# Optimization experiments

Measured on AMD Instinct MI355X. Metric: run time of the kernel, lower is better.

The kernel has to match this reference:

```python
import jax, jax.numpy as jnp
import numpy as np

TEMPERATURE = 0.75
SINKHORN_ITERS = 7
EPS = 1e-6
R_THRESH = 1e-3


def setup_inputs() -> dict:
    key = jax.random.key(0)
    k1, k2, k3, k4 = jax.random.split(key, 4)
    b, h, t, d = 1, 8, 2048, 64
    n = 32  # uniform buckets of size t // n = 64
    q = jax.random.normal(k1, (b, h, t, d), jnp.float32)
    k_ = jax.random.normal(k2, (b, h, t, d), jnp.float32)
    v = jax.random.normal(k3, (b, h, t, d), jnp.float32)
    gumbel_u = jax.random.uniform(k4, (b * h, n, n), jnp.float32)
    return {"q": q, "k": k_, "v": v, "gumbel_u": gumbel_u, "num_buckets": n}


def _sort_net_R(qm, km, gumbel_u, d):
    # qm, km: [bh, n, s, d] -> bucket sums [bh, n, d]
    q_sums = qm.sum(axis=2)
    k_sums = km.sum(axis=2)
    logits = jnp.einsum('bie,bje->bij', q_sums, k_sums) * (d ** -0.5)
    # gumbel_sinkhorn(relu(logits))
    r = jnp.log(jax.nn.relu(logits) + EPS)
    g = -jnp.log(-jnp.log(gumbel_u + EPS) + EPS)
    r = (r + g) / TEMPERATURE
    for _ in range(SINKHORN_ITERS):
        r = r - jax.nn.logsumexp(r, axis=2, keepdims=True)
        r = r - jax.nn.logsumexp(r, axis=1, keepdims=True)
    return jnp.exp(r)  # [bh, n, n]


def reference(q, k, v, gumbel_u, num_buckets):
    b, h, t, d = q.shape
    bh = b * h
    n = num_buckets
    s = t // n  # uniform bucket size
    qm = q.reshape(bh, n, s, d)
    km = k.reshape(bh, n, s, d)
    vm = v.reshape(bh, n, s, d)

    R = _sort_net_R(qm, km, gumbel_u, d)
    # torch skips pairs with R_ij <= 1e-3 (output is zero); multiply by masked R
    Rm = jnp.where(R > R_THRESH, R, 0.0)

    scale = d ** -0.5
    # keys for pair (i, j) are concat(k_i, k_j): split score into self + cross
    S_self = jnp.einsum('bise,bite->bist', qm, km) * scale          # [bh,n,s,s]
    S_cross = jnp.einsum('bise,bjte->bijst', qm, km) * scale        # [bh,n,n,s,s]
    scores = jnp.concatenate(
        [jnp.broadcast_to(S_self[:, :, None], (bh, n, n, s, s)), S_cross],
        axis=-1)                                                    # [bh,n,n,s,2s]
    w = jax.nn.softmax(scores, axis=-1)
    w_i, w_j = w[..., :s], w[..., s:]
    # out_ij = (w_i @ v_i + w_j @ v_j) * R_ij, summed over j
    out = (jnp.einsum('bijst,bite,bij->bise', w_i, vm, Rm)
           + jnp.einsum('bijst,bjte,bij->bise', w_j, vm, Rm))       # [bh,n,s,d]
    return out.reshape(b, h, t, d)
```

## Files before the change

kernel.cpp:

```cpp
#include <hip/hip_runtime.h>
#include <math.h>
#include <stdint.h>

#define BH 8
#define NB 32
#define SS 64
#define DD 64
#define TT 2048

typedef float f32x16 __attribute__((ext_vector_type(16)));
typedef short bf16x8 __attribute__((ext_vector_type(8)));
typedef unsigned short u16;

__device__ __forceinline__ unsigned pkbf(float a, float b) {
  unsigned r;
  asm("v_cvt_pk_bf16_f32 %0, %1, %2" : "=v"(r) : "v"(a), "v"(b));
  return r;
}
__device__ __forceinline__ float exp2x(float x) {
  float r;
  asm("v_exp_f32 %0, %1" : "=v"(r) : "v"(x));
  return r;
}
__device__ __forceinline__ float log2x(float x) {
  float r;
  asm("v_log_f32 %0, %1" : "=v"(r) : "v"(x));
  return r;
}
__device__ __forceinline__ float bfhi(unsigned u16v) {
  union { unsigned u; float f; } x;
  x.u = u16v << 16;
  return x.f;
}
__device__ __forceinline__ bf16x8 pack8v(const f32x16& v, const int b) {
  union { unsigned u[4]; bf16x8 v8; } x;
  x.u[0] = pkbf(v[b + 0], v[b + 1]);
  x.u[1] = pkbf(v[b + 2], v[b + 3]);
  x.u[2] = pkbf(v[b + 4], v[b + 5]);
  x.u[3] = pkbf(v[b + 6], v[b + 7]);
  return x.v8;
}

__global__ __launch_bounds__(256) void prep_kernel(
    const float* __restrict__ q, const float* __restrict__ k, const float* __restrict__ v,
    u16* __restrict__ qb, u16* __restrict__ kb, u16* __restrict__ vtb,
    float* __restrict__ qsum, float* __restrict__ ksum)
{
  __shared__ float qt[64][68];
  __shared__ float kt[64][68];
  __shared__ float vt[64][68];

  const int T = blockIdx.x;
  const int t = threadIdx.x;
  const float* qsrc = q + (size_t)T * 4096;
  const float* ksrc = k + (size_t)T * 4096;
  const float* vsrc = v + (size_t)T * 4096;

#pragma unroll
  for (int r4 = 0; r4 < 4; ++r4) {
    int f = r4 * 256 + t;
    int row = f >> 4, c4 = (f & 15) << 2;
    *(float4*)&qt[row][c4] = ((const float4*)qsrc)[f];
    *(float4*)&kt[row][c4] = ((const float4*)ksrc)[f];
    *(float4*)&vt[row][c4] = ((const float4*)vsrc)[f];
  }
  __syncthreads();

  const float qscale = 0.18033688011112042f;

#pragma unroll
  for (int half = 0; half < 2; ++half) {
    int x = half * 256 + t;
    int c = x >> 6, lane = x & 63;
    int l31 = lane & 31, hi = lane >> 5;
    int m = c >> 2, s = c & 3;
    int row = l31 + 32 * m;
    int cb = 16 * s + 4 * hi;
    float4 a = *(const float4*)&qt[row][cb];
    float4 b = *(const float4*)&qt[row][cb + 8];
    uint4 o;
    o.x = pkbf(a.x * qscale, a.y * qscale);
    o.y = pkbf(a.z * qscale, a.w * qscale);
    o.z = pkbf(b.x * qscale, b.y * qscale);
    o.w = pkbf(b.z * qscale, b.w * qscale);
    *(uint4*)(qb + (size_t)T * 4096 + (size_t)x * 8) = o;

    float4 ka = *(const float4*)&kt[row][cb];
    float4 kb4 = *(const float4*)&kt[row][cb + 8];
    uint4 ko;
    ko.x = pkbf(ka.x, ka.y);
    ko.y = pkbf(ka.z, ka.w);
    ko.z = pkbf(kb4.x, kb4.y);
    ko.w = pkbf(kb4.z, kb4.w);
    *(uint4*)(kb + (size_t)T * 4096 + (size_t)x * 8) = ko;

    int d = l31 + 32 * m;
    int kb0 = 16 * s + 4 * hi;
    uint4 vo;
    vo.x = pkbf(vt[kb0 + 0][d], vt[kb0 + 1][d]);
    vo.y = pkbf(vt[kb0 + 2][d], vt[kb0 + 3][d]);
    vo.z = pkbf(vt[kb0 + 8][d], vt[kb0 + 9][d]);
    vo.w = pkbf(vt[kb0 + 10][d], vt[kb0 + 11][d]);
    *(uint4*)(vtb + (size_t)T * 4096 + (size_t)x * 8) = vo;
  }

  if (t < 64) {
    float s = 0.f;
#pragma unroll 8
    for (int r = 0; r < 64; ++r) s += qt[r][t];
    qsum[T * 64 + t] = s;
  } else if (t < 128) {
    int c = t - 64;
    float s = 0.f;
#pragma unroll 8
    for (int r = 0; r < 64; ++r) s += kt[r][c];
    ksum[T * 64 + c] = s;
  }
}

__global__ __launch_bounds__(512) void attn_kernel(
    const u16* __restrict__ qb, const u16* __restrict__ kb,
    const u16* __restrict__ vtb, const float* __restrict__ qsum,
    const float* __restrict__ ksum, const float* __restrict__ gu,
    float* __restrict__ out)
{
  __shared__ __align__(16) unsigned char smem[35840];
  float (*redh)[2][32][68] = (float (*)[2][32][68])smem;
  float (*cbuf)[32] = (float (*)[32])(smem + 34816);
  float* qs = (float*)smem;
  float* ks = qs + 32 * 65;
  float* LT = ks + 32 * 65;

  const int bh  = blockIdx.x & 7;
  const int i   = blockIdx.x >> 3;
  const int t   = threadIdx.x;
  const int w   = t >> 6;
  const int n   = w & 1;
  const int g   = w >> 1;
  const int lane = t & 63;
  const int l31 = lane & 31;
  const int hi  = lane >> 5;

  const u16* qtile = qb + ((size_t)(bh * NB + i)) * 4096;
  const u16* kbh   = kb + (size_t)bh * NB * 4096;
  const u16* vbh   = vtb + (size_t)bh * NB * 4096;

#define LOADG(dst, base)                                                      \
  {                                                                           \
    _Pragma("unroll") for (int m = 0; m < 2; ++m)                             \
    _Pragma("unroll") for (int s = 0; s < 4; ++s)                             \
      dst[m][s] = *(const bf16x8*)((base) + ((size_t)((m * 4 + s) * 64 + lane)) * 8); \
  }

  bf16x8 qB[4];
#pragma unroll
  for (int s = 0; s < 4; ++s)
    qB[s] = *(const bf16x8*)(qtile + ((size_t)((n * 4 + s) * 64 + lane)) * 8);
  bf16x8 kA[2][4], vB[2][4], kAi[2][4];
  LOADG(kA, kbh + (size_t)g * 4096);
  LOADG(vB, vbh + (size_t)g * 4096);
  LOADG(kAi, kbh + (size_t)i * 4096);

  float rij8[8];
  {
    const float L2E = 1.4426950408889634f;
    const float LN2 = 0.6931471805599453f;

    if (t < 256) {
      int idx = t * 8;
      float4 a = *(const float4*)(qsum + bh * 2048 + idx);
      float4 b = *(const float4*)(qsum + bh * 2048 + idx + 4);
      float4 c = *(const float4*)(ksum + bh * 2048 + idx);
      float4 d = *(const float4*)(ksum + bh * 2048 + idx + 4);
      int bkt = idx >> 6, e = idx & 63;
      float* qd = qs + bkt * 65 + e;
      qd[0] = a.x; qd[1] = a.y; qd[2] = a.z; qd[3] = a.w;
      qd[4] = b.x; qd[5] = b.y; qd[6] = b.z; qd[7] = b.w;
      float* kd = ks + bkt * 65 + e;
      kd[0] = c.x; kd[1] = c.y; kd[2] = c.z; kd[3] = c.w;
      kd[4] = d.x; kd[5] = d.y; kd[6] = d.z; kd[7] = d.w;
    }
    __syncthreads();

    if (t < 64) {
      bf16x8 qh[4], ql[4], kh[4], kl[4];
#pragma unroll
      for (int s = 0; s < 4; ++s) {
        const int base = 16 * s + 4 * hi;
        float qv[8], kv[8];
#pragma unroll
        for (int x = 0; x < 8; ++x) {
          int off = (x & 3) + 8 * (x >> 2);
          qv[x] = qs[l31 * 65 + base + off];
          kv[x] = ks[l31 * 65 + base + off];
        }
        union { unsigned u[4]; bf16x8 v8; } qhh, qll, khh, kll;
#pragma unroll
        for (int p = 0; p < 4; ++p) {
          unsigned hq = pkbf(qv[2 * p], qv[2 * p + 1]);
          qhh.u[p] = hq;
          qll.u[p] = pkbf(qv[2 * p] - bfhi(hq & 0xffffu),
                          qv[2 * p + 1] - bfhi(hq >> 16));
          unsigned hk = pkbf(kv[2 * p], kv[2 * p + 1]);
          khh.u[p] = hk;
          kll.u[p] = pkbf(kv[2 * p] - bfhi(hk & 0xffffu),
                          kv[2 * p + 1] - bfhi(hk >> 16));
        }
        qh[s] = qhh.v8; ql[s] = qll.v8;
        kh[s] = khh.v8; kl[s] = kll.v8;
      }
      f32x16 accL;
#pragma unroll
      for (int r = 0; r < 16; ++r) accL[r] = 0.f;
#pragma unroll
      for (int s = 0; s < 4; ++s) {
        accL = __builtin_amdgcn_mfma_f32_32x32x16_bf16(qh[s], kh[s], accL, 0, 0, 0);
        accL = __builtin_amdgcn_mfma_f32_32x32x16_bf16(qh[s], kl[s], accL, 0, 0, 0);
        accL = __builtin_amdgcn_mfma_f32_32x32x16_bf16(ql[s], kh[s], accL, 0, 0, 0);
      }
#pragma unroll
      for (int r = 0; r < 16; ++r) {
        int ii = (r & 3) + 8 * (r >> 2) + 4 * hi;
        float L = accL[r] * 0.125f;
        float u = gu[bh * 1024 + ii * 32 + l31];
        float il = log2x(u + 1e-6f) * LN2;
        float gg = -(log2x(-il + 1e-6f) * LN2);
        float lr = log2x(fmaxf(L, 0.f) + 1e-6f) * LN2;
        LT[ii * 33 + l31] = (lr + gg) * (1.0f / 0.75f);
      }
    }
    __syncthreads();

    if (t < 64) {
      const int l = t;
      const int half16 = (l & 1) * 16;
      const int major = l >> 1;
      float r[16];
#pragma unroll
      for (int x = 0; x < 16; ++x) r[x] = LT[major * 33 + half16 + x];

      for (int it = 0; it < 7; ++it) {
        {
          float e[16];
#pragma unroll
          for (int x = 0; x < 16; ++x) e[x] = exp2x(r[x] * L2E);
#pragma unroll
          for (int off = 8; off > 0; off >>= 1)
#pragma unroll
            for (int x = 0; x < off; ++x) e[x] += e[x + off];
          float s = e[0] + __shfl_xor(e[0], 1, 64);
          float L = log2x(fmaxf(s, 1e-30f)) * LN2;
#pragma unroll
          for (int x = 0; x < 16; ++x) r[x] -= L;
        }
#pragma unroll
        for (int x = 0; x < 16; ++x) LT[major * 33 + half16 + x] = r[x];
#pragma unroll
        for (int x = 0; x < 16; ++x) r[x] = LT[(half16 + x) * 33 + major];
        {
          float e[16];
#pragma unroll
          for (int x = 0; x < 16; ++x) e[x] = exp2x(r[x] * L2E);
#pragma unroll
          for (int off = 8; off > 0; off >>= 1)
#pragma unroll
            for (int x = 0; x < off; ++x) e[x] += e[x + off];
          float s = e[0] + __shfl_xor(e[0], 1, 64);
          float L = log2x(fmaxf(s, 1e-30f)) * LN2;
#pragma unroll
          for (int x = 0; x < 16; ++x) r[x] -= L;
        }
        if (it < 6) {
#pragma unroll
          for (int x = 0; x < 16; ++x) LT[(half16 + x) * 33 + major] = r[x];
#pragma unroll
          for (int x = 0; x < 16; ++x) r[x] = LT[major * 33 + half16 + x];
        }
      }

#pragma unroll
      for (int x = 0; x < 16; ++x) {
        float R = exp2x(r[x] * L2E);
        LT[(half16 + x) * 33 + major] = (R > 1e-3f) ? R : 0.f;
      }
    }
    __syncthreads();

#pragma unroll
    for (int jj = 0; jj < 8; ++jj) rij8[jj] = LT[i * 33 + g + 4 * jj];
  }

  float m0, S0;
  bf16x8 psA[4];
  {
    f32x16 aS0, aS1;
#pragma unroll
    for (int r = 0; r < 16; ++r) { aS0[r] = 0.f; aS1[r] = 0.f; }
#pragma unroll
    for (int s = 0; s < 4; ++s) {
      aS0 = __builtin_amdgcn_mfma_f32_32x32x16_bf16(kAi[0][s], qB[s], aS0, 0, 0, 0);
      aS1 = __builtin_amdgcn_mfma_f32_32x32x16_bf16(kAi[1][s], qB[s], aS1, 0, 0, 0);
    }
    float mx[16];
#pragma unroll
    for (int r = 0; r < 16; ++r) mx[r] = fmaxf(aS0[r], aS1[r]);
#pragma unroll
    for (int off = 8; off > 0; off >>= 1)
#pragma unroll
      for (int r = 0; r < off; ++r) mx[r] = fmaxf(mx[r], mx[r + off]);
    float mm = fmaxf(mx[0], __shfl_xor(mx[0], 32, 64));
#pragma unroll
    for (int r = 0; r < 16; ++r) { aS0[r] = exp2x(aS0[r] - mm); aS1[r] = exp2x(aS1[r] - mm); }
    float sm[16];
#pragma unroll
    for (int r = 0; r < 16; ++r) sm[r] = aS0[r] + aS1[r];
#pragma unroll
    for (int off = 8; off > 0; off >>= 1)
#pragma unroll
      for (int r = 0; r < off; ++r) sm[r] += sm[r + off];
    S0 = sm[0] + __shfl_xor(sm[0], 32, 64);
    m0 = mm;
    psA[0] = pack8v(aS0, 0);
    psA[1] = pack8v(aS0, 8);
    psA[2] = pack8v(aS1, 0);
    psA[3] = pack8v(aS1, 8);
  }

  f32x16 outAcc[2];
#pragma unroll
  for (int nv = 0; nv < 2; ++nv)
#pragma unroll
    for (int e = 0; e < 16; ++e) outAcc[nv][e] = 0.f;
  float cacc = 0.f;

#pragma unroll
  for (int jj = 0; jj < 8; ++jj) {
    const int j = g + 4 * jj;
    const float rij = rij8[jj];

    f32x16 a0, a1;
#pragma unroll
    for (int r = 0; r < 16; ++r) { a0[r] = 0.f; a1[r] = 0.f; }
    __builtin_amdgcn_s_setprio(1);
#pragma unroll
    for (int s = 0; s < 4; ++s) {
      a0 = __builtin_amdgcn_mfma_f32_32x32x16_bf16(kA[0][s], qB[s], a0, 0, 0, 0);
      a1 = __builtin_amdgcn_mfma_f32_32x32x16_bf16(kA[1][s], qB[s], a1, 0, 0, 0);
    }
    __builtin_amdgcn_s_setprio(0);

    if (jj < 7) LOADG(kA, kbh + (size_t)(j + 4) * 4096);

    float mx[16];
#pragma unroll
    for (int r = 0; r < 16; ++r) mx[r] = fmaxf(a0[r], a1[r]);
#pragma unroll
    for (int off = 8; off > 0; off >>= 1)
#pragma unroll
      for (int r = 0; r < off; ++r) mx[r] = fmaxf(mx[r], mx[r + off]);
    float mc = fmaxf(mx[0], __shfl_xor(mx[0], 32, 64));
    float mj = fmaxf(m0, mc);
#pragma unroll
    for (int r = 0; r < 16; ++r) { a0[r] = exp2x(a0[r] - mj); a1[r] = exp2x(a1[r] - mj); }
    float sm[16];
#pragma unroll
    for (int r = 0; r < 16; ++r) sm[r] = a0[r] + a1[r];
#pragma unroll
    for (int off = 8; off > 0; off >>= 1)
#pragma unroll
      for (int r = 0; r < off; ++r) sm[r] += sm[r + off];
    float ssum = sm[0] + __shfl_xor(sm[0], 32, 64);
    float e0 = exp2x(m0 - mj);
    float den = S0 * e0 + ssum;
    float inv = rij / den;
    cacc += e0 * inv;
#pragma unroll
    for (int r = 0; r < 16; ++r) { a0[r] *= inv; a1[r] *= inv; }

    __builtin_amdgcn_s_setprio(1);
#pragma unroll
    for (int s = 0; s < 4; ++s) {
      bf16x8 wf = (s < 2) ? pack8v(a0, 8 * (s & 1)) : pack8v(a1, 8 * (s & 1));
      outAcc[0] = __builtin_amdgcn_mfma_f32_32x32x16_bf16(wf, vB[0][s], outAcc[0], 0, 0, 0);
      outAcc[1] = __builtin_amdgcn_mfma_f32_32x32x16_bf16(wf, vB[1][s], outAcc[1], 0, 0, 0);
    }
    __builtin_amdgcn_s_setprio(0);

    if (jj < 7) LOADG(vB, vbh + (size_t)(j + 4) * 4096);
  }

  {
    const u16* vib = vbh + (size_t)i * 4096;
    bf16x8 vBi[2][4];
    LOADG(vBi, vib);
    f32x16 U[2];
#pragma unroll
    for (int nv = 0; nv < 2; ++nv)
#pragma unroll
      for (int e = 0; e < 16; ++e) U[nv][e] = 0.f;
#pragma unroll
    for (int s = 0; s < 4; ++s) {
      U[0] = __builtin_amdgcn_mfma_f32_32x32x16_bf16(psA[s], vBi[0][s], U[0], 0, 0, 0);
      U[1] = __builtin_amdgcn_mfma_f32_32x32x16_bf16(psA[s], vBi[1][s], U[1], 0, 0, 0);
    }
    if (hi == 0) cbuf[w][l31] = cacc;
    __syncthreads();
#pragma unroll
    for (int r = 0; r < 16; ++r) {
      int row = (r & 3) + 8 * (r >> 2) + 4 * hi;
      float cr = cbuf[w][row];
      outAcc[0][r] += U[0][r] * cr;
      outAcc[1][r] += U[1][r] * cr;
    }
  }

#define RED_W(buf)                                                         \
  {                                                                        \
    _Pragma("unroll") for (int ne = 0; ne < 2; ++ne)                       \
    _Pragma("unroll") for (int r = 0; r < 16; ++r) {                       \
      int row = (r & 3) + 8 * (r >> 2) + 4 * hi;                           \
      (buf)[row][l31 + 32 * ne] = outAcc[ne][r];                           \
    }                                                                      \
  }
#define RED_A(buf)                                                         \
  {                                                                        \
    _Pragma("unroll") for (int ne = 0; ne < 2; ++ne)                       \
    _Pragma("unroll") for (int r = 0; r < 16; ++r) {                       \
      int row = (r & 3) + 8 * (r >> 2) + 4 * hi;                           \
      outAcc[ne][r] += (buf)[row][l31 + 32 * ne];                          \
    }                                                                      \
  }

  if (g >= 2) RED_W(redh[n][g - 2]);
  __syncthreads();
  if (g < 2) RED_A(redh[n][g]);
  __syncthreads();
  if (g == 1) RED_W(redh[n][0]);
  __syncthreads();
  if (g == 0) {
    RED_A(redh[n][0]);
    RED_W(redh[n][0]);
  }
  __syncthreads();

  {
    int row = t >> 3;
    int nr = row >> 5, lrow = row & 31;
    int col0 = (t & 7) * 8;
    float4 a = *(const float4*)&redh[nr][0][lrow][col0];
    float4 b = *(const float4*)&redh[nr][0][lrow][col0 + 4];
    float* ob = out + ((size_t)bh * TT + i * SS + row) * DD + col0;
    *(float4*)ob = a;
    *(float4*)(ob + 4) = b;
  }
#undef LOADG
#undef RED_W
#undef RED_A
}

extern "C" void kernel_launch(void* const* d_in, const int* in_sizes, int n_in,
                              void* d_out, int out_size, void* d_ws, size_t ws_size,
                              hipStream_t stream) {
  (void)in_sizes; (void)n_in; (void)out_size; (void)ws_size;
  const float* q  = (const float*)d_in[0];
  const float* k  = (const float*)d_in[1];
  const float* v  = (const float*)d_in[2];
  const float* gu = (const float*)d_in[3];
  float* out = (float*)d_out;

  char* wsb = (char*)d_ws;
  u16* qb   = (u16*)(wsb);
  u16* kb   = (u16*)(wsb + (1 << 21));
  u16* vtb  = (u16*)(wsb + (2 << 21));
  float* qsum = (float*)(wsb + (3 << 21));
  float* ksum = (float*)(wsb + (3 << 21) + (1 << 16));

  prep_kernel<<<256, 256, 0, stream>>>(q, k, v, qb, kb, vtb, qsum, ksum);
  attn_kernel<<<BH * NB, 512, 0, stream>>>(qb, kb, vtb, qsum, ksum, gu, out);
}
```

Baseline: 32.88 us.

## Split each query bucket's two row halves across separate blocks, 8 j-groups per block

The attention grid doubles so each block handles one 32-row half of a query bucket. Inside a block, all 8 waves now split the 32 key buckets into strided groups of 4, instead of 2 row halves times 4 groups of 8. The cross-wave reduction gains more stages (8 to 1 tree) and the output write shrinks to one float4 per thread. The aim is more blocks to fill the CUs and shorter per-wave loops. In exchange, every block redoes the Sinkhorn sort-net computation, which doubles that redundant work, and the reduction adds extra barriers. launch_bounds(512,4) also caps registers, which risks spills.

Result: slower. 105.1 us (+219.7%).

```diff
diff --git a/kernel.cpp b/kernel.cpp
--- a/kernel.cpp
+++ b/kernel.cpp
@@ -118,25 +118,25 @@
   }
 }
 
-__global__ __launch_bounds__(512) void attn_kernel(
+__global__ __launch_bounds__(512, 4) void attn_kernel(
     const u16* __restrict__ qb, const u16* __restrict__ kb,
     const u16* __restrict__ vtb, const float* __restrict__ qsum,
     const float* __restrict__ ksum, const float* __restrict__ gu,
     float* __restrict__ out)
 {
   __shared__ __align__(16) unsigned char smem[35840];
-  float (*redh)[2][32][68] = (float (*)[2][32][68])smem;
+  float (*redh)[32][68] = (float (*)[32][68])smem;
   float (*cbuf)[32] = (float (*)[32])(smem + 34816);
   float* qs = (float*)smem;
   float* ks = qs + 32 * 65;
   float* LT = ks + 32 * 65;
 
   const int bh  = blockIdx.x & 7;
-  const int i   = blockIdx.x >> 3;
+  const int i   = (blockIdx.x >> 3) & 31;
+  const int n   = blockIdx.x >> 8;
   const int t   = threadIdx.x;
   const int w   = t >> 6;
-  const int n   = w & 1;
-  const int g   = w >> 1;
+  const int g   = w;
   const int lane = t & 63;
   const int l31 = lane & 31;
   const int hi  = lane >> 5;
@@ -161,7 +161,7 @@
   LOADG(vB, vbh + (size_t)g * 4096);
   LOADG(kAi, kbh + (size_t)i * 4096);
 
-  float rij8[8];
+  float rij4[4];
   {
     const float L2E = 1.4426950408889634f;
     const float LN2 = 0.6931471805599453f;
@@ -287,7 +287,7 @@
     __syncthreads();
 
 #pragma unroll
-    for (int jj = 0; jj < 8; ++jj) rij8[jj] = LT[i * 33 + g + 4 * jj];
+    for (int jj = 0; jj < 4; ++jj) rij4[jj] = LT[i * 33 + g + 8 * jj];
   }
 
   float m0, S0;
@@ -334,9 +334,9 @@
   float cacc = 0.f;
 
 #pragma unroll
-  for (int jj = 0; jj < 8; ++jj) {
-    const int j = g + 4 * jj;
-    const float rij = rij8[jj];
+  for (int jj = 0; jj < 4; ++jj) {
+    const int j = g + 8 * jj;
+    const float rij = rij4[jj];
 
     f32x16 a0, a1;
 #pragma unroll
@@ -349,7 +349,7 @@
     }
     __builtin_amdgcn_s_setprio(0);
 
-    if (jj < 7) LOADG(kA, kbh + (size_t)(j + 4) * 4096);
+    if (jj < 3) LOADG(kA, kbh + (size_t)(j + 8) * 4096);
 
     float mx[16];
 #pragma unroll
@@ -386,7 +386,7 @@
     }
     __builtin_amdgcn_s_setprio(0);
 
-    if (jj < 7) LOADG(vB, vbh + (size_t)(j + 4) * 4096);
+    if (jj < 3) LOADG(vB, vbh + (size_t)(j + 8) * 4096);
   }
 
   {
@@ -431,27 +431,28 @@
     }                                                                      \
   }
 
-  if (g >= 2) RED_W(redh[n][g - 2]);
-  __syncthreads();
-  if (g < 2) RED_A(redh[n][g]);
-  __syncthreads();
-  if (g == 1) RED_W(redh[n][0]);
-  __syncthreads();
-  if (g == 0) {
-    RED_A(redh[n][0]);
-    RED_W(redh[n][0]);
+  if (w >= 4) RED_W(redh[w - 4]);
+  __syncthreads();
+  if (w < 4) RED_A(redh[w]);
+  __syncthreads();
+  if (w == 2 || w == 3) RED_W(redh[w - 2]);
+  __syncthreads();
+  if (w < 2) RED_A(redh[w]);
+  __syncthreads();
+  if (w == 1) RED_W(redh[0]);
+  __syncthreads();
+  if (w == 0) {
+    RED_A(redh[0]);
+    RED_W(redh[0]);
   }
   __syncthreads();
 
   {
-    int row = t >> 3;
-    int nr = row >> 5, lrow = row & 31;
-    int col0 = (t & 7) * 8;
-    float4 a = *(const float4*)&redh[nr][0][lrow][col0];
-    float4 b = *(const float4*)&redh[nr][0][lrow][col0 + 4];
-    float* ob = out + ((size_t)bh * TT + i * SS + row) * DD + col0;
+    int row = t >> 4;
+    int col0 = (t & 15) * 4;
+    float4 a = *(const float4*)&redh[0][row][col0];
+    float* ob = out + ((size_t)bh * TT + i * SS + n * 32 + row) * DD + col0;
     *(float4*)ob = a;
-    *(float4*)(ob + 4) = b;
   }
 #undef LOADG
 #undef RED_W
@@ -476,5 +477,5 @@
   float* ksum = (float*)(wsb + (3 << 21) + (1 << 16));
 
   prep_kernel<<<256, 256, 0, stream>>>(q, k, v, qb, kb, vtb, qsum, ksum);
-  attn_kernel<<<BH * NB, 512, 0, stream>>>(qb, kb, vtb, qsum, ksum, gu, out);
-}
+  attn_kernel<<<2 * BH * NB, 512, 0, stream>>>(qb, kb, vtb, qsum, ksum, gu, out);
+}
```
